# Kernel tuning notes

Measured on AMD Instinct MI355X. Metric: run time of the kernel, lower is better.

The kernel has to match this reference:

```python
import jax, jax.numpy as jnp
import numpy as np


def setup_inputs() -> dict:
    key = jax.random.key(0)
    k1, k2 = jax.random.split(key)
    B, N, M, D = 4, 8192, 8192, 3
    preds = jax.random.normal(k1, (B, M, D), dtype=jnp.float32)
    gts = jax.random.normal(k2, (B, N, D), dtype=jnp.float32)
    return {"preds": preds, "gts": gts, "c": 1}


def reference(preds, gts, c):
    # x = gts [B, Nx, D], y = preds [B, Ny, D] (matches batch_pairwise_dist(gts, preds))
    x, y = gts, preds
    cf = jnp.asarray(c, dtype=x.dtype)
    # P[b, i, j] = ||x_i||^2 + ||y_j||^2 - 2 <x_i, y_j>  (squared Euclidean distance)
    zz = jnp.einsum('bnd,bmd->bnm', x, y)            # [B, Nx, Ny]
    rx = jnp.sum(x * x, axis=-1)[:, :, None]          # [B, Nx, 1]
    ry = jnp.sum(y * y, axis=-1)[:, None, :]          # [B, 1, Ny]
    P = rx + ry - 2.0 * zz                            # [B, Nx, Ny]

    def huber(v):
        return jnp.where(v < cf, 0.5 * v * v, cf * v - 0.5 * cf * cf)

    loss_1 = jnp.sum(huber(jnp.min(P, axis=1)))       # min over Nx (gts side)
    loss_2 = jnp.sum(huber(jnp.min(P, axis=2)))       # min over Ny (preds side)
    return loss_1 + loss_2
```

## Files before the change

### kernel.cpp

```cpp
#include <hip/hip_runtime.h>
#include <math.h>

typedef _Float16 f16x8 __attribute__((ext_vector_type(8)));
typedef float f32x16 __attribute__((ext_vector_type(16)));

#define TILE 1024

__device__ __forceinline__ float decode_scalar(const int* p) {
    int i = *p;
    if (i > -16777216 && i < 16777216) return (float)i;
    return __int_as_float(i);
}
__device__ __forceinline__ float min3f(float a, float b, float c) {
    float d;
    asm("v_min3_f32 %0, %1, %2, %3" : "=v"(d) : "v"(a), "v"(b), "v"(c));
    return d;
}

__device__ __forceinline__ f16x8 make_afrag(float x, float y, float z, int half) {
    const float rn = fmaf(x, x, fmaf(y, y, z * z));
    const float ax = -2.f * x, ay = -2.f * y, az = -2.f * z;
    const _Float16 ahx = (_Float16)ax, ahy = (_Float16)ay, ahz = (_Float16)az;
    const _Float16 alx = (_Float16)(ax - (float)ahx);
    const _Float16 aly = (_Float16)(ay - (float)ahy);
    const _Float16 alz = (_Float16)(az - (float)ahz);
    const _Float16 rh = (_Float16)rn, rl = (_Float16)(rn - (float)rh);
    const _Float16 one = (_Float16)1.f;
    if (half == 0) return (f16x8){ahx, ahy, ahz, alx, aly, alz, ahx, ahy};
    return (f16x8){ahz, alx, aly, alz, rh, rl, one, one};
}
__device__ __forceinline__ void make_bfrags(float x, float y, float z,
                                            f16x8* b0, f16x8* b1) {
    const float rn = fmaf(x, x, fmaf(y, y, z * z));
    const _Float16 bhx = (_Float16)x, bhy = (_Float16)y, bhz = (_Float16)z;
    const _Float16 blx = (_Float16)(x - (float)bhx);
    const _Float16 bly = (_Float16)(y - (float)bhy);
    const _Float16 blz = (_Float16)(z - (float)bhz);
    const _Float16 rh = (_Float16)rn, rl = (_Float16)(rn - (float)rh);
    const _Float16 one = (_Float16)1.f;
    *b0 = (f16x8){bhx, bhy, bhz, bhx, bhy, bhz, blx, bly};
    *b1 = (f16x8){blz, blx, bly, blz, one, one, rh, rl};
}

__global__ __launch_bounds__(256) void nn_mfma(
    const float* __restrict__ preds, const float* __restrict__ gts,
    int M, int N, int B, int rsplit, int Qstride, float* __restrict__ part)
{
    const int zc    = blockIdx.z;
    const int dir   = zc / rsplit;
    const int chunk = zc - dir * rsplit;
    const int b     = blockIdx.y;

    const int Q = dir ? N : M;
    const int R = dir ? M : N;
    const float* __restrict__ qraw = (dir ? gts : preds) + (size_t)b * Q * 3;
    const float* __restrict__ rraw = (dir ? preds : gts) + (size_t)b * R * 3;

    const int q0blk = blockIdx.x * 256;
    if (q0blk >= Q) return;
    const int tid  = threadIdx.x;
    const int lane = tid & 63, w = tid >> 6;
    const int q0   = q0blk + w * 64;
    const int lrow = lane & 31, lh = lane >> 5;

    float ax = 0.f, ay = 0.f, az = 0.f, bx = 0.f, by = 0.f, bz = 0.f;
    const int qa = q0 + lrow, qb = q0 + 32 + lrow;
    if (qa < Q) { const float* s = qraw + (size_t)qa * 3; ax = s[0]; ay = s[1]; az = s[2]; }
    if (qb < Q) { const float* s = qraw + (size_t)qb * 3; bx = s[0]; by = s[1]; bz = s[2]; }
    const f16x8 af0 = make_afrag(ax, ay, az, lh);
    const f16x8 af1 = make_afrag(bx, by, bz, lh);

    __shared__ f16x8 sB[TILE * 2];

    f32x16 rm0, rm1;
    #pragma unroll
    for (int j = 0; j < 16; ++j) { rm0[j] = INFINITY; rm1[j] = INFINITY; }

    const int tilesTotal = (R + TILE - 1) / TILE;
    const int tpc = (tilesTotal + rsplit - 1) / rsplit;
    const int t0 = chunk * tpc;
    const int t1 = min(tilesTotal, t0 + tpc);

    for (int tt = t0; tt < t1; ++tt) {
        const int s0 = tt * TILE;
        __syncthreads();
        #pragma unroll
        for (int k = 0; k < 4; ++k) {
            const int p  = tid + k * 256;
            const int gi = s0 + p;
            f16x8 b0, b1;
            if (gi < R) {
                const float* s = rraw + (size_t)gi * 3;
                make_bfrags(s[0], s[1], s[2], &b0, &b1);
            } else {
                const _Float16 z0 = (_Float16)0.f, one = (_Float16)1.f;
                const _Float16 big = (_Float16)60000.f;
                b0 = (f16x8){z0, z0, z0, z0, z0, z0, z0, z0};
                b1 = (f16x8){z0, z0, z0, z0, one, one, big, z0};
            }
            const int g = p >> 5, sl = p & 31;
            sB[g * 64 + sl]      = b0;
            sB[g * 64 + 32 + sl] = b1;
        }
        __syncthreads();

        #pragma unroll 1
        for (int tp = 0; tp < TILE / 64; ++tp) {
            const f16x8 cb0 = sB[2 * tp * 64 + lane];
            const f16x8 cb1 = sB[(2 * tp + 1) * 64 + lane];
            f32x16 d00, d01, d10, d11;
            asm volatile(
                "v_mfma_f32_32x32x16_f16 %0, %4, %6, 0\n\t"
                "v_mfma_f32_32x32x16_f16 %1, %4, %7, 0\n\t"
                "v_mfma_f32_32x32x16_f16 %2, %5, %6, 0\n\t"
                "v_mfma_f32_32x32x16_f16 %3, %5, %7, 0\n\t"
                "s_nop 7\n\t"
                "s_nop 7\n\t"
                "s_nop 7\n\t"
                "s_nop 7"
                : "=&v"(d00), "=&v"(d01), "=&v"(d10), "=&v"(d11)
                : "v"(af0), "v"(af1), "v"(cb0), "v"(cb1));
            #pragma unroll
            for (int j = 0; j < 16; ++j) rm0[j] = min3f(d00[j], d01[j], rm0[j]);
            #pragma unroll
            for (int j = 0; j < 16; ++j) rm1[j] = min3f(d10[j], d11[j], rm1[j]);
        }
    }

    __syncthreads();
    float* sT = (float*)&sB[0] + (w << 11);
    const int c  = lrow;
    const int sw = 4 * (c & 7);

    #pragma unroll
    for (int jj = 0; jj < 4; ++jj) {
        const int qb0 = jj * 8 + 4 * lh;
        float4 v0 = { rm0[4*jj], rm0[4*jj+1], rm0[4*jj+2], rm0[4*jj+3] };
        *(float4*)&sT[c * 64 + (qb0 ^ sw)] = v0;
        const int qb1 = 32 + qb0;
        float4 v1 = { rm1[4*jj], rm1[4*jj+1], rm1[4*jj+2], rm1[4*jj+3] };
        *(float4*)&sT[c * 64 + (qb1 ^ sw)] = v1;
    }
    __syncthreads();

    float t16[16];
    #pragma unroll
    for (int cc = 0; cc < 16; ++cc) {
        const float va = sT[(2*cc)     * 64 + (lane ^ (4 * ((2*cc)     & 7)))];
        const float vb = sT[(2*cc + 1) * 64 + (lane ^ (4 * ((2*cc + 1) & 7)))];
        t16[cc] = fminf(va, vb);
    }
    #pragma unroll
    for (int s = 8; s > 0; s >>= 1)
        #pragma unroll
        for (int i = 0; i < 8; ++i)
            if (i < s) t16[i] = fminf(t16[i], t16[i + s]);

    const size_t pbase = (((size_t)dir * B + b) * rsplit + chunk) * (size_t)Qstride + q0;
    part[pbase + lane] = t16[0];
}

__global__ __launch_bounds__(1024) void huber_reduce(
    const float* __restrict__ part, const int* __restrict__ cptr,
    int M, int N, int B, int rsplit, int Qstride, float* __restrict__ out)
{
    const int dir = blockIdx.z;
    const int b   = blockIdx.y;
    const int Q   = dir ? N : M;
    const int tid = threadIdx.x;
    const int j   = blockIdx.x * 1024 + tid;

    float h = 0.f;
    if (j < Q) {
        const size_t base = (((size_t)dir * B + b) * rsplit) * (size_t)Qstride + j;
        float v = part[base];
        #pragma unroll 4
        for (int k = 1; k < rsplit; ++k) v = fminf(v, part[base + (size_t)k * Qstride]);
        const float c = decode_scalar(cptr);
        h = (v < c) ? (0.5f * v * v) : fmaf(c, v, -0.5f * c * c);
    }

    #pragma unroll
    for (int off = 32; off > 0; off >>= 1) h += __shfl_down(h, off, 64);

    __shared__ float wsum[16];
    if ((tid & 63) == 0) wsum[tid >> 6] = h;
    __syncthreads();
    if (tid < 64) {
        float t = (tid < 16) ? wsum[tid] : 0.f;
        #pragma unroll
        for (int off = 8; off > 0; off >>= 1) t += __shfl_down(t, off, 64);
        if (tid == 0) atomicAdd(out, t);
    }
}

extern "C" void kernel_launch(void* const* d_in, const int* in_sizes, int n_in,
                              void* d_out, int out_size, void* d_ws, size_t ws_size,
                              hipStream_t stream) {
    const float* preds = (const float*)d_in[0];
    const float* gts   = (const float*)d_in[1];
    const int*   cptr  = (const int*)d_in[2];

    const int B = 4, D = 3;
    const int M = in_sizes[0] / (B * D);
    const int N = in_sizes[1] / (B * D);
    const int Qmax = (M > N) ? M : N;
    const int Qstride = (Qmax + 255) & ~255;
    const int rsplit = 4;

    float* part = (float*)d_ws;
    hipMemsetAsync(d_out, 0, (size_t)out_size * sizeof(float), stream);

    dim3 g1(Qstride / 256, B, 2 * rsplit);
    nn_mfma<<<g1, 256, 0, stream>>>(preds, gts, M, N, B, rsplit, Qstride, part);

    dim3 g2((Qmax + 1023) / 1024, B, 2);
    huber_reduce<<<g2, 1024, 0, stream>>>(part, cptr, M, N, B, rsplit, Qstride,
                                          (float*)d_out);
}
```

Baseline: 32.56 us.

## Software-pipeline MFMA issue with min folding to hide MFMA latency

Restructures the inner tile loop so two MFMAs for the next B fragment are issued while the previous results are folded into the running minima. This removes the s_nop padding that stalled every iteration, overlapping MFMA latency with VALU min work and LDS loads. In exchange, min3 becomes min2, so more VALU min instructions are issued, and more accumulator registers are live. It also relies on the dependency spacing between MFMA writes and VALU reads being enough without explicit nops.

```diff
diff --git a/kernel.cpp b/kernel.cpp
--- a/kernel.cpp
+++ b/kernel.cpp
@@ -11,9 +11,9 @@
     if (i > -16777216 && i < 16777216) return (float)i;
     return __int_as_float(i);
 }
-__device__ __forceinline__ float min3f(float a, float b, float c) {
+__device__ __forceinline__ float min2f(float a, float b) {
     float d;
-    asm("v_min3_f32 %0, %1, %2, %3" : "=v"(d) : "v"(a), "v"(b), "v"(c));
+    asm("v_min_f32 %0, %1, %2" : "=v"(d) : "v"(a), "v"(b));
     return d;
 }
 
@@ -41,6 +41,25 @@
     *b0 = (f16x8){bhx, bhy, bhz, bhx, bhy, bhz, blx, bly};
     *b1 = (f16x8){blz, blx, bly, blz, one, one, rh, rl};
 }
+
+#define MFMA2(D0, D1, CB)                                            \
+    asm volatile(                                                    \
+        "v_mfma_f32_32x32x16_f16 %0, %2, %4, 0\n\t"                  \
+        "v_mfma_f32_32x32x16_f16 %1, %3, %4, 0"                      \
+        : "=&v"(D0), "=&v"(D1) : "v"(af0), "v"(af1), "v"(CB))
+
+#define MFMA2N(D0, D1, CB)                                           \
+    asm volatile(                                                    \
+        "v_mfma_f32_32x32x16_f16 %0, %2, %4, 0\n\t"                  \
+        "v_mfma_f32_32x32x16_f16 %1, %3, %4, 0\n\t"                  \
+        "s_nop 7\n\ts_nop 7\n\ts_nop 7\n\ts_nop 7"                   \
+        : "=&v"(D0), "=&v"(D1) : "v"(af0), "v"(af1), "v"(CB))
+
+#define FOLD(D0, D1)                                                 \
+    _Pragma("unroll")                                                \
+    for (int j = 0; j < 16; ++j) rm0[j] = min2f(rm0[j], D0[j]);      \
+    _Pragma("unroll")                                                \
+    for (int j = 0; j < 16; ++j) rm1[j] = min2f(rm1[j], D1[j]);
 
 __global__ __launch_bounds__(256) void nn_mfma(
     const float* __restrict__ preds, const float* __restrict__ gts,
@@ -104,27 +123,24 @@
         }
         __syncthreads();
 
+        const f16x8* pl = sB + lane;
+        f16x8 cbA = pl[0];
+        f16x8 cbB = pl[64];
+        f32x16 d0a, d1a, d0b, d1b;
+        MFMA2N(d0a, d1a, cbA);
+
         #pragma unroll 1
-        for (int tp = 0; tp < TILE / 64; ++tp) {
-            const f16x8 cb0 = sB[2 * tp * 64 + lane];
-            const f16x8 cb1 = sB[(2 * tp + 1) * 64 + lane];
-            f32x16 d00, d01, d10, d11;
-            asm volatile(
-                "v_mfma_f32_32x32x16_f16 %0, %4, %6, 0\n\t"
-                "v_mfma_f32_32x32x16_f16 %1, %4, %7, 0\n\t"
-                "v_mfma_f32_32x32x16_f16 %2, %5, %6, 0\n\t"
-                "v_mfma_f32_32x32x16_f16 %3, %5, %7, 0\n\t"
-                "s_nop 7\n\t"
-                "s_nop 7\n\t"
-                "s_nop 7\n\t"
-                "s_nop 7"
-                : "=&v"(d00), "=&v"(d01), "=&v"(d10), "=&v"(d11)
-                : "v"(af0), "v"(af1), "v"(cb0), "v"(cb1));
-            #pragma unroll
-            for (int j = 0; j < 16; ++j) rm0[j] = min3f(d00[j], d01[j], rm0[j]);
-            #pragma unroll
-            for (int j = 0; j < 16; ++j) rm1[j] = min3f(d10[j], d11[j], rm1[j]);
+        for (int s = 0; s < 15; ++s) {
+            MFMA2(d0b, d1b, cbB);
+            cbA = pl[(2 * s + 2) * 64];
+            FOLD(d0a, d1a)
+            MFMA2(d0a, d1a, cbA);
+            cbB = pl[(2 * s + 3) * 64];
+            FOLD(d0b, d1b)
         }
+        MFMA2N(d0b, d1b, cbB);
+        FOLD(d0a, d1a)
+        FOLD(d0b, d1b)
     }
 
     __syncthreads();
```

Result: slower. 36.73 us (+12.8%).
